# Kernel optimization log

Measured on AMD Instinct MI355X. Metric: run time of the kernel, lower is better.

## Reference

```python
import jax, jax.numpy as jnp
import numpy as np

N = 50000
E = 800000
DIN = 128
DH = [128, 128]
DOUT = 64


def setup_inputs() -> dict:
    key = jax.random.key(0)
    ks = jax.random.split(key, 12)

    def w(k, fan_in, fan_out):
        return jax.random.normal(k, (fan_in, fan_out), dtype=jnp.float32) / np.sqrt(fan_in)

    x = jax.random.normal(ks[0], (N, DIN), dtype=jnp.float32)
    edge_index = jax.random.randint(ks[1], (2, E), 0, N, dtype=jnp.int64)
    return {
        "x": x,
        "edge_index": edge_index,
        # SAGEConv layer 0: lin_l (aggregated neighbors, with bias), lin_r (root, no bias)
        "Wl0": w(ks[2], DIN, DH[0]), "Wr0": w(ks[3], DIN, DH[0]), "b0": jnp.zeros((DH[0],), jnp.float32),
        # SAGEConv layer 1
        "Wl1": w(ks[4], DH[0], DH[1]), "Wr1": w(ks[5], DH[0], DH[1]), "b1": jnp.zeros((DH[1],), jnp.float32),
        # final Linear
        "Wout": w(ks[6], DH[1], DOUT), "bout": jnp.zeros((DOUT,), jnp.float32),
    }


def sage_conv(h, src, dst, Wl, Wr, b):
    # mean-aggregate source features at destination nodes
    msg = h[src]                                                  # [E, d]
    agg = jax.ops.segment_sum(msg, dst, num_segments=N)           # [N, d]
    cnt = jax.ops.segment_sum(jnp.ones((src.shape[0],), h.dtype), dst, num_segments=N)
    agg = agg / jnp.maximum(cnt, 1.0)[:, None]
    return agg @ Wl + h @ Wr + b


def reference(x, edge_index, Wl0, Wr0, b0, Wl1, Wr1, b1, Wout, bout):
    src, dst = edge_index[0], edge_index[1]
    h = jax.nn.relu(sage_conv(x, src, dst, Wl0, Wr0, b0))
    # dropout: identity in eval mode
    h = jax.nn.relu(sage_conv(h, src, dst, Wl1, Wr1, b1))
    out = h @ Wout + bout                                         # [N, DOUT]
    return jax.nn.softmax(out, axis=1)
```

## Files before the change

### kernel.cpp

```cpp
#include <hip/hip_runtime.h>


#define CAP 64

typedef __attribute__((ext_vector_type(8))) short bf16x8;
typedef __attribute__((ext_vector_type(4))) float f32x4;

__device__ __forceinline__ unsigned short bf16_rtne(float f) {
    unsigned u = __float_as_uint(f);
    u += 0x7FFFu + ((u >> 16) & 1u);
    return (unsigned short)(u >> 16);
}

__device__ __forceinline__ void pack_w_body(const float* __restrict__ Wl,
                                            const float* __restrict__ Wr,
                                            unsigned short* __restrict__ Wp, int i) {
    int j = i & 7;
    int l = (i >> 3) & 63;
    int ntile = (i >> 9) & 7;
    int kstep = i >> 12;
    int k = kstep * 32 + (l >> 4) * 8 + j;
    int n = ntile * 16 + (l & 15);
    float v = (k < 128) ? Wl[k * 128 + n] : Wr[(k - 128) * 128 + n];
    Wp[i] = bf16_rtne(v);
}

__global__ __launch_bounds__(256) void build_prep_kernel(
        const int* __restrict__ src, const int* __restrict__ dst,
        int* __restrict__ cnt, unsigned short* __restrict__ csr,
        int E, int N, int fillBlocks,
        const float* __restrict__ x, unsigned short* __restrict__ xb, int n4, int cvtBlocks,
        const float* __restrict__ Wl0, const float* __restrict__ Wr0,
        unsigned short* __restrict__ Wp1,
        const float* __restrict__ Wl1, const float* __restrict__ Wr1,
        unsigned short* __restrict__ Wp2,
        const float* __restrict__ Wout, unsigned short* __restrict__ Wpo) {
    int b = blockIdx.x;
    if (b < fillBlocks) {
        int xcd = b & 7;
        int chunk = b >> 3;
        int Nper = (N + 7) >> 3;
        int dLo = xcd * Nper;
        int dHi = min(dLo + Nper, N);
        int e0 = chunk * 1024 + (int)threadIdx.x * 4;
        if (e0 + 3 < E) {
            int4 d4 = *(const int4*)(dst + e0);
            int4 s4 = *(const int4*)(src + e0);
            int dd[4] = {d4.x, d4.y, d4.z, d4.w};
            int ss[4] = {s4.x, s4.y, s4.z, s4.w};
            int pos[4];
#pragma unroll
            for (int u = 0; u < 4; ++u)
                pos[u] = (dd[u] >= dLo && dd[u] < dHi) ? atomicAdd(&cnt[dd[u]], 1) : CAP;
#pragma unroll
            for (int u = 0; u < 4; ++u) {
                if (pos[u] < CAP) {
                    int s = ((unsigned)ss[u] < (unsigned)N) ? ss[u] : 0;
                    csr[dd[u] * CAP + pos[u]] = (unsigned short)s;
                }
            }
        } else {
            for (int e = e0; e < E; ++e) {
                int d = dst[e];
                if (d >= dLo && d < dHi) {
                    int p = atomicAdd(&cnt[d], 1);
                    if (p < CAP) {
                        int s = src[e];
                        csr[d * CAP + p] =
                            (unsigned short)(((unsigned)s < (unsigned)N) ? s : 0);
                    }
                }
            }
        }
    } else if (b < fillBlocks + cvtBlocks) {
        int i = (b - fillBlocks) * 256 + (int)threadIdx.x;
        if (i < n4) {
            float4 v = ((const float4*)x)[i];
            ushort4 o;
            o.x = bf16_rtne(v.x); o.y = bf16_rtne(v.y);
            o.z = bf16_rtne(v.z); o.w = bf16_rtne(v.w);
            ((ushort4*)xb)[i] = o;
        }
    } else if (b < fillBlocks + cvtBlocks + 128) {
        pack_w_body(Wl0, Wr0, Wp1, (b - fillBlocks - cvtBlocks) * 256 + (int)threadIdx.x);
    } else if (b < fillBlocks + cvtBlocks + 256) {
        pack_w_body(Wl1, Wr1, Wp2, (b - fillBlocks - cvtBlocks - 128) * 256 + (int)threadIdx.x);
    } else {
        int i = (b - fillBlocks - cvtBlocks - 256) * 256 + (int)threadIdx.x;
        int j = i & 7;
        int l = (i >> 3) & 63;
        int nt = (i >> 9) & 3;
        int ks = i >> 11;
        int k = ks * 32 + (l >> 4) * 8 + j;
        int n = nt * 16 + (l & 15);
        Wpo[i] = bf16_rtne(Wout[k * 64 + n]);
    }
}

__global__ __launch_bounds__(256) void agg_bf16_kernel(
        const unsigned short* __restrict__ hb, const int* __restrict__ cnt,
        const unsigned short* __restrict__ csr, unsigned short* __restrict__ aggb, int N) {
    int t = blockIdx.x * blockDim.x + threadIdx.x;
    int node = t >> 5;
    int lane = t & 31;
    if (node >= N) return;
    int deg = min(cnt[node], CAP);
    int s0 = node * CAP;
    int s1 = s0 + deg;
    const uint2* h2 = (const uint2*)hb;
    float a0 = 0.f, a1 = 0.f, a2 = 0.f, a3 = 0.f;
    for (int base = 0; base < deg; base += 32) {
        int nc = min(32, deg - base);
        int e = min(s0 + base + lane, s1 - 1);
        int idx = csr[e];
        for (int j = 0; j < nc; j += 8) {
            uint2 v[8];
#pragma unroll
            for (int u = 0; u < 8; ++u) {
                int sidx = __shfl(idx, j + u, 32);
                v[u] = h2[(size_t)sidx * 32 + lane];
            }
#pragma unroll
            for (int u = 0; u < 8; ++u) {
                unsigned vx = (j + u < nc) ? v[u].x : 0u;
                unsigned vy = (j + u < nc) ? v[u].y : 0u;
                a0 += __uint_as_float(vx << 16);
                a1 += __uint_as_float(vx & 0xFFFF0000u);
                a2 += __uint_as_float(vy << 16);
                a3 += __uint_as_float(vy & 0xFFFF0000u);
            }
        }
    }
    float inv = 1.0f / (float)max(deg, 1);
    ushort4 o;
    o.x = bf16_rtne(a0 * inv); o.y = bf16_rtne(a1 * inv);
    o.z = bf16_rtne(a2 * inv); o.w = bf16_rtne(a3 * inv);
    ((ushort4*)aggb)[(size_t)node * 32 + lane] = o;
}

__device__ __forceinline__ void mfma_dual_gemm(
        const unsigned short* __restrict__ aggb, const unsigned short* __restrict__ rootb,
        const unsigned short* __restrict__ Wp, int rowc, int quad, int lane,
        f32x4 acc[8]) {
#pragma unroll
    for (int t = 0; t < 8; ++t) acc[t] = (f32x4){0.f, 0.f, 0.f, 0.f};
    for (int ks = 0; ks < 8; ++ks) {
        const unsigned short* Abase = (ks < 4) ? aggb : rootb;
        int kloc = (ks & 3) * 32 + quad * 8;
        bf16x8 a = *(const bf16x8*)(Abase + (size_t)rowc * 128 + kloc);
#pragma unroll
        for (int t = 0; t < 8; ++t) {
            bf16x8 bf = *(const bf16x8*)(Wp + ((size_t)(ks * 8 + t) * 64 + lane) * 8);
            acc[t] = __builtin_amdgcn_mfma_f32_16x16x32_bf16(a, bf, acc[t], 0, 0, 0);
        }
    }
}

__global__ __launch_bounds__(256) void mfma_layer1_kernel(
        const unsigned short* __restrict__ aggb, const unsigned short* __restrict__ rootb,
        const unsigned short* __restrict__ Wp, const float* __restrict__ b,
        unsigned short* __restrict__ houtb, int N) {
    int lane = threadIdx.x & 63;
    int wv = threadIdx.x >> 6;
    int m0 = blockIdx.x * 64 + wv * 16;
    int quad = lane >> 4;
    int rowc = min(m0 + (lane & 15), N - 1);
    f32x4 acc[8];
    mfma_dual_gemm(aggb, rootb, Wp, rowc, quad, lane, acc);
    int colb = lane & 15;
#pragma unroll
    for (int t = 0; t < 8; ++t) {
        int col = t * 16 + colb;
        float bias = b[col];
#pragma unroll
        for (int r = 0; r < 4; ++r) {
            int node = m0 + quad * 4 + r;
            if (node < N) {
                float v = fmaxf(acc[t][r] + bias, 0.f);
                houtb[(size_t)node * 128 + col] = bf16_rtne(v);
            }
        }
    }
}

__global__ __launch_bounds__(256) void mfma_layer2_out_kernel(
        const unsigned short* __restrict__ aggb, const unsigned short* __restrict__ rootb,
        const unsigned short* __restrict__ Wp, const float* __restrict__ b,
        const unsigned short* __restrict__ Wpo, const float* __restrict__ bout,
        float* __restrict__ out, int N) {
    __shared__ unsigned short sH[4][16 * 128];
    int lane = threadIdx.x & 63;
    int wv = threadIdx.x >> 6;
    int m0 = blockIdx.x * 64 + wv * 16;
    int quad = lane >> 4;
    int c = lane & 15;
    int rowc = min(m0 + c, N - 1);
    f32x4 acc[8];
    mfma_dual_gemm(aggb, rootb, Wp, rowc, quad, lane, acc);
#pragma unroll
    for (int t = 0; t < 8; ++t) {
        int col = t * 16 + c;
        float bias = b[col];
#pragma unroll
        for (int r = 0; r < 4; ++r) {
            sH[wv][(quad * 4 + r) * 128 + col] = bf16_rtne(fmaxf(acc[t][r] + bias, 0.f));
        }
    }
    __syncthreads();

    f32x4 acc2[4];
#pragma unroll
    for (int nt = 0; nt < 4; ++nt) acc2[nt] = (f32x4){0.f, 0.f, 0.f, 0.f};
#pragma unroll
    for (int ks = 0; ks < 4; ++ks) {
        bf16x8 a = *(const bf16x8*)&sH[wv][c * 128 + ks * 32 + quad * 8];
#pragma unroll
        for (int nt = 0; nt < 4; ++nt) {
            bf16x8 bf = *(const bf16x8*)(Wpo + ((size_t)(ks * 4 + nt) * 64 + lane) * 8);
            acc2[nt] = __builtin_amdgcn_mfma_f32_16x16x32_bf16(a, bf, acc2[nt], 0, 0, 0);
        }
    }

    float bo[4];
#pragma unroll
    for (int nt = 0; nt < 4; ++nt) bo[nt] = bout[nt * 16 + c];
#pragma unroll
    for (int r = 0; r < 4; ++r) {
        float v[4];
#pragma unroll
        for (int nt = 0; nt < 4; ++nt) v[nt] = acc2[nt][r] + bo[nt];
        float m = fmaxf(fmaxf(v[0], v[1]), fmaxf(v[2], v[3]));
#pragma unroll
        for (int ofs = 1; ofs < 16; ofs <<= 1) m = fmaxf(m, __shfl_xor(m, ofs, 64));
        float e[4];
        float s = 0.f;
#pragma unroll
        for (int nt = 0; nt < 4; ++nt) { e[nt] = __expf(v[nt] - m); s += e[nt]; }
#pragma unroll
        for (int ofs = 1; ofs < 16; ofs <<= 1) s += __shfl_xor(s, ofs, 64);
        float inv = 1.0f / s;
        int node = m0 + quad * 4 + r;
        if (node < N) {
#pragma unroll
            for (int nt = 0; nt < 4; ++nt)
                out[(size_t)node * 64 + nt * 16 + c] = e[nt] * inv;
        }
    }
}

extern "C" void kernel_launch(void* const* d_in, const int* in_sizes, int n_in,
                              void* d_out, int out_size, void* d_ws, size_t ws_size,
                              hipStream_t stream) {
    const float* x    = (const float*)d_in[0];
    const int*   ei   = (const int*)d_in[1];
    const float* Wl0  = (const float*)d_in[2];
    const float* Wr0  = (const float*)d_in[3];
    const float* b0   = (const float*)d_in[4];
    const float* Wl1  = (const float*)d_in[5];
    const float* Wr1  = (const float*)d_in[6];
    const float* b1   = (const float*)d_in[7];
    const float* Wout = (const float*)d_in[8];
    const float* bout = (const float*)d_in[9];

    int N = in_sizes[0] / 128;
    int E = in_sizes[1] / 2;
    const int* src = ei;
    const int* dst = ei + E;

    char* p = (char*)d_ws;
    auto alloc = [&](size_t bytes) -> char* {
        char* r = p;
        p += (bytes + 255) & ~(size_t)255;
        return r;
    };
    int*            cnt  = (int*)alloc((size_t)N * 4);
    unsigned short* csr  = (unsigned short*)alloc((size_t)N * CAP * 2);
    unsigned short* xb   = (unsigned short*)alloc((size_t)N * 128 * 2);
    unsigned short* h0b  = (unsigned short*)alloc((size_t)N * 128 * 2);
    unsigned short* aggb = (unsigned short*)alloc((size_t)N * 128 * 2);
    unsigned short* Wp1  = (unsigned short*)alloc((size_t)32768 * 2);
    unsigned short* Wp2  = (unsigned short*)alloc((size_t)32768 * 2);
    unsigned short* Wpo  = (unsigned short*)alloc((size_t)8192 * 2);

    hipMemsetAsync(cnt, 0, (size_t)N * 4, stream);

    int n4 = N * 128 / 4;
    int cvtBlocks = (n4 + 255) / 256;
    int chunks = (E + 1023) / 1024;
    int fillBlocks = chunks * 8;
    build_prep_kernel<<<fillBlocks + cvtBlocks + 256 + 32, 256, 0, stream>>>(
        src, dst, cnt, csr, E, N, fillBlocks,
        x, xb, n4, cvtBlocks, Wl0, Wr0, Wp1, Wl1, Wr1, Wp2, Wout, Wpo);

    int ab = (N * 32 + 255) / 256;
    int gb = (N + 63) / 64;

    agg_bf16_kernel<<<ab, 256, 0, stream>>>(xb, cnt, csr, aggb, N);
    mfma_layer1_kernel<<<gb, 256, 0, stream>>>(aggb, xb, Wp1, b0, h0b, N);
    agg_bf16_kernel<<<ab, 256, 0, stream>>>(h0b, cnt, csr, aggb, N);
    mfma_layer2_out_kernel<<<gb, 256, 0, stream>>>(aggb, h0b, Wp2, b1,
                                                   Wpo, bout, (float*)d_out, N);
}
```

Before: 216.8 us.

## Build CSR via two-pass bucket sort instead of global atomics per edge

Replaces the per-edge global atomicAdd CSR fill, which had every XCD re-read all edges, with a two-pass bucketing scheme. Edges are first bucketed by dst>>8 in shared memory and scattered to per-XCD global bucket buffers. A new kernel then builds the CSR for each 256-node bucket in LDS and writes it out coalesced. This cuts global atomics and redundant edge reads, at the cost of an extra kernel launch, fixed bucket capacities (BCAP8=768) that can silently drop edges, and 16-bit packing that assumes fewer than 65536 nodes.

Result: faster. 198.0 us (-8.6%).

```diff
diff --git a/kernel.cpp b/kernel.cpp
--- a/kernel.cpp
+++ b/kernel.cpp
@@ -2,6 +2,9 @@
 
 
 #define CAP 64
+#define NBK 256
+#define EPB 2048
+#define BCAP8 768
 
 typedef __attribute__((ext_vector_type(8))) short bf16x8;
 typedef __attribute__((ext_vector_type(4))) float f32x4;
@@ -25,10 +28,10 @@
     Wp[i] = bf16_rtne(v);
 }
 
-__global__ __launch_bounds__(256) void build_prep_kernel(
+__global__ __launch_bounds__(256) void bucket_prep_kernel(
         const int* __restrict__ src, const int* __restrict__ dst,
-        int* __restrict__ cnt, unsigned short* __restrict__ csr,
-        int E, int N, int fillBlocks,
+        unsigned int* __restrict__ gtail, unsigned int* __restrict__ gbuf,
+        int E, int aBlocks,
         const float* __restrict__ x, unsigned short* __restrict__ xb, int n4, int cvtBlocks,
         const float* __restrict__ Wl0, const float* __restrict__ Wr0,
         unsigned short* __restrict__ Wp1,
@@ -36,44 +39,80 @@
         unsigned short* __restrict__ Wp2,
         const float* __restrict__ Wout, unsigned short* __restrict__ Wpo) {
     int b = blockIdx.x;
-    if (b < fillBlocks) {
+    if (b < aBlocks) {
+        __shared__ unsigned int hist[NBK];
+        __shared__ unsigned int pref[NBK + 1];
+        __shared__ int baseS[NBK];
+        __shared__ unsigned int scat[EPB];
+        __shared__ unsigned char scatb[EPB];
+        int tid = (int)threadIdx.x;
         int xcd = b & 7;
-        int chunk = b >> 3;
-        int Nper = (N + 7) >> 3;
-        int dLo = xcd * Nper;
-        int dHi = min(dLo + Nper, N);
-        int e0 = chunk * 1024 + (int)threadIdx.x * 4;
-        if (e0 + 3 < E) {
-            int4 d4 = *(const int4*)(dst + e0);
-            int4 s4 = *(const int4*)(src + e0);
-            int dd[4] = {d4.x, d4.y, d4.z, d4.w};
-            int ss[4] = {s4.x, s4.y, s4.z, s4.w};
-            int pos[4];
-#pragma unroll
-            for (int u = 0; u < 4; ++u)
-                pos[u] = (dd[u] >= dLo && dd[u] < dHi) ? atomicAdd(&cnt[dd[u]], 1) : CAP;
-#pragma unroll
-            for (int u = 0; u < 4; ++u) {
-                if (pos[u] < CAP) {
-                    int s = ((unsigned)ss[u] < (unsigned)N) ? ss[u] : 0;
-                    csr[dd[u] * CAP + pos[u]] = (unsigned short)s;
-                }
-            }
+        hist[tid] = 0u;
+        __syncthreads();
+
+        int e0 = b * EPB + tid * 8;
+        int dd[8], ss[8], bb[8];
+        unsigned rr[8];
+        bool vld[8];
+        if (e0 + 7 < E) {
+            int4 d0 = *(const int4*)(dst + e0);
+            int4 d1 = *(const int4*)(dst + e0 + 4);
+            int4 s0 = *(const int4*)(src + e0);
+            int4 s1 = *(const int4*)(src + e0 + 4);
+            dd[0] = d0.x; dd[1] = d0.y; dd[2] = d0.z; dd[3] = d0.w;
+            dd[4] = d1.x; dd[5] = d1.y; dd[6] = d1.z; dd[7] = d1.w;
+            ss[0] = s0.x; ss[1] = s0.y; ss[2] = s0.z; ss[3] = s0.w;
+            ss[4] = s1.x; ss[5] = s1.y; ss[6] = s1.z; ss[7] = s1.w;
+#pragma unroll
+            for (int u = 0; u < 8; ++u) vld[u] = true;
         } else {
-            for (int e = e0; e < E; ++e) {
-                int d = dst[e];
-                if (d >= dLo && d < dHi) {
-                    int p = atomicAdd(&cnt[d], 1);
-                    if (p < CAP) {
-                        int s = src[e];
-                        csr[d * CAP + p] =
-                            (unsigned short)(((unsigned)s < (unsigned)N) ? s : 0);
-                    }
-                }
-            }
-        }
-    } else if (b < fillBlocks + cvtBlocks) {
-        int i = (b - fillBlocks) * 256 + (int)threadIdx.x;
+#pragma unroll
+            for (int u = 0; u < 8; ++u) {
+                int e = e0 + u;
+                vld[u] = (e < E);
+                dd[u] = vld[u] ? dst[e] : 0;
+                ss[u] = vld[u] ? src[e] : 0;
+            }
+        }
+#pragma unroll
+        for (int u = 0; u < 8; ++u) {
+            bb[u] = dd[u] >> 8;
+            rr[u] = vld[u] ? atomicAdd(&hist[bb[u]], 1u) : 0u;
+        }
+        __syncthreads();
+        pref[tid + 1] = hist[tid];
+        if (tid == 0) pref[0] = 0u;
+        __syncthreads();
+        for (int off = 1; off < NBK; off <<= 1) {
+            unsigned add = (tid + 1 > off) ? pref[tid + 1 - off] : 0u;
+            __syncthreads();
+            pref[tid + 1] += add;
+            __syncthreads();
+        }
+        {
+            unsigned h = hist[tid];
+            unsigned gb0 = (h != 0u) ? atomicAdd(&gtail[xcd * NBK + tid], h) : 0u;
+            baseS[tid] = (int)((unsigned)(xcd * NBK + tid) * BCAP8 + gb0) - (int)pref[tid];
+        }
+        __syncthreads();
+#pragma unroll
+        for (int u = 0; u < 8; ++u) {
+            if (vld[u]) {
+                unsigned idx = pref[bb[u]] + rr[u];
+                scat[idx] = ((unsigned)dd[u] << 16) | (unsigned)(ss[u] & 0xFFFF);
+                scatb[idx] = (unsigned char)bb[u];
+            }
+        }
+        __syncthreads();
+        unsigned tot = pref[NBK];
+        for (unsigned i = (unsigned)tid; i < tot; i += 256u) {
+            int bk = (int)scatb[i];
+            int gi = baseS[bk] + (int)i;
+            unsigned segBase = (unsigned)(xcd * NBK + bk) * BCAP8;
+            if ((unsigned)gi - segBase < BCAP8) gbuf[gi] = scat[i];
+        }
+    } else if (b < aBlocks + cvtBlocks) {
+        int i = (b - aBlocks) * 256 + (int)threadIdx.x;
         if (i < n4) {
             float4 v = ((const float4*)x)[i];
             ushort4 o;
@@ -81,12 +120,12 @@
             o.z = bf16_rtne(v.z); o.w = bf16_rtne(v.w);
             ((ushort4*)xb)[i] = o;
         }
-    } else if (b < fillBlocks + cvtBlocks + 128) {
-        pack_w_body(Wl0, Wr0, Wp1, (b - fillBlocks - cvtBlocks) * 256 + (int)threadIdx.x);
-    } else if (b < fillBlocks + cvtBlocks + 256) {
-        pack_w_body(Wl1, Wr1, Wp2, (b - fillBlocks - cvtBlocks - 128) * 256 + (int)threadIdx.x);
+    } else if (b < aBlocks + cvtBlocks + 128) {
+        pack_w_body(Wl0, Wr0, Wp1, (b - aBlocks - cvtBlocks) * 256 + (int)threadIdx.x);
+    } else if (b < aBlocks + cvtBlocks + 256) {
+        pack_w_body(Wl1, Wr1, Wp2, (b - aBlocks - cvtBlocks - 128) * 256 + (int)threadIdx.x);
     } else {
-        int i = (b - fillBlocks - cvtBlocks - 256) * 256 + (int)threadIdx.x;
+        int i = (b - aBlocks - cvtBlocks - 256) * 256 + (int)threadIdx.x;
         int j = i & 7;
         int l = (i >> 3) & 63;
         int nt = (i >> 9) & 3;
@@ -95,6 +134,35 @@
         int n = nt * 16 + (l & 15);
         Wpo[i] = bf16_rtne(Wout[k * 64 + n]);
     }
+}
+
+__global__ __launch_bounds__(256) void fill_csr_kernel(
+        const unsigned int* __restrict__ gtail, const unsigned int* __restrict__ gbuf,
+        int* __restrict__ cnt, unsigned short* __restrict__ csr, int N) {
+    __shared__ unsigned int cntL[256];
+    __shared__ unsigned short stage[256 * CAP];
+    int b = blockIdx.x;
+    int tid = (int)threadIdx.x;
+    cntL[tid] = 0u;
+    __syncthreads();
+#pragma unroll 1
+    for (int xcd = 0; xcd < 8; ++xcd) {
+        unsigned nE = gtail[xcd * NBK + b];
+        if (nE > BCAP8) nE = BCAP8;
+        const unsigned int* g = gbuf + (size_t)(xcd * NBK + b) * BCAP8;
+        for (unsigned i = (unsigned)tid; i < nE; i += 256u) {
+            unsigned pk = g[i];
+            int dl = (int)((pk >> 16) & 255u);
+            unsigned p = atomicAdd(&cntL[dl], 1u);
+            if (p < CAP) stage[dl * CAP + p] = (unsigned short)(pk & 0xFFFFu);
+        }
+    }
+    __syncthreads();
+    const uint4* s4 = (const uint4*)stage;
+    uint4* g4 = (uint4*)(csr + (size_t)b * (256 * CAP));
+    for (int i = tid; i < (256 * CAP) / 8; i += 256) g4[i] = s4[i];
+    int node = b * 256 + tid;
+    if (node < N) cnt[node] = (int)cntL[tid];
 }
 
 __global__ __launch_bounds__(256) void agg_bf16_kernel(
@@ -266,6 +334,7 @@
     int E = in_sizes[1] / 2;
     const int* src = ei;
     const int* dst = ei + E;
+    int nb = (N + 255) >> 8;
 
     char* p = (char*)d_ws;
     auto alloc = [&](size_t bytes) -> char* {
@@ -273,24 +342,27 @@
         p += (bytes + 255) & ~(size_t)255;
         return r;
     };
-    int*            cnt  = (int*)alloc((size_t)N * 4);
-    unsigned short* csr  = (unsigned short*)alloc((size_t)N * CAP * 2);
-    unsigned short* xb   = (unsigned short*)alloc((size_t)N * 128 * 2);
-    unsigned short* h0b  = (unsigned short*)alloc((size_t)N * 128 * 2);
-    unsigned short* aggb = (unsigned short*)alloc((size_t)N * 128 * 2);
-    unsigned short* Wp1  = (unsigned short*)alloc((size_t)32768 * 2);
-    unsigned short* Wp2  = (unsigned short*)alloc((size_t)32768 * 2);
-    unsigned short* Wpo  = (unsigned short*)alloc((size_t)8192 * 2);
-
-    hipMemsetAsync(cnt, 0, (size_t)N * 4, stream);
+    unsigned int*   gtail = (unsigned int*)alloc((size_t)8 * NBK * 4);
+    unsigned int*   gbuf  = (unsigned int*)alloc((size_t)8 * NBK * BCAP8 * 4);
+    int*            cnt   = (int*)alloc((size_t)N * 4);
+    unsigned short* csr   = (unsigned short*)alloc((size_t)nb * 256 * CAP * 2);
+    unsigned short* xb    = (unsigned short*)alloc((size_t)N * 128 * 2);
+    unsigned short* h0b   = (unsigned short*)alloc((size_t)N * 128 * 2);
+    unsigned short* aggb  = (unsigned short*)alloc((size_t)N * 128 * 2);
+    unsigned short* Wp1   = (unsigned short*)alloc((size_t)32768 * 2);
+    unsigned short* Wp2   = (unsigned short*)alloc((size_t)32768 * 2);
+    unsigned short* Wpo   = (unsigned short*)alloc((size_t)8192 * 2);
+
+    hipMemsetAsync(gtail, 0, (size_t)8 * NBK * 4, stream);
 
     int n4 = N * 128 / 4;
     int cvtBlocks = (n4 + 255) / 256;
-    int chunks = (E + 1023) / 1024;
-    int fillBlocks = chunks * 8;
-    build_prep_kernel<<<fillBlocks + cvtBlocks + 256 + 32, 256, 0, stream>>>(
-        src, dst, cnt, csr, E, N, fillBlocks,
+    int aBlocks = (E + EPB - 1) / EPB;
+    bucket_prep_kernel<<<aBlocks + cvtBlocks + 256 + 32, 256, 0, stream>>>(
+        src, dst, gtail, gbuf, E, aBlocks,
         x, xb, n4, cvtBlocks, Wl0, Wr0, Wp1, Wl1, Wr1, Wp2, Wout, Wpo);
+
+    fill_csr_kernel<<<nb, 256, 0, stream>>>(gtail, gbuf, cnt, csr, N);
 
     int ab = (N * 32 + 255) / 256;
     int gb = (N + 63) / 64;
```
